# Performance work log

Measured on AMD Instinct MI355X. Metric: run time of the kernel, lower is better.

## Reference

```python
import jax, jax.numpy as jnp
import numpy as np

B, LQ, LK, QD, KD, VD, H = 8, 128, 1024, 128, 128, 128, 128
NEG_INF = -1e6  # d2l masked_softmax fill value


def setup_inputs() -> dict:
    key = jax.random.key(0)
    k1, k2, k3, k4, k5, k6, k7 = jax.random.split(key, 7)
    return {
        "queries": jax.random.normal(k1, (B, LQ, QD), dtype=jnp.float32),
        "keys": jax.random.normal(k2, (B, LK, KD), dtype=jnp.float32),
        "values": jax.random.normal(k3, (B, LK, VD), dtype=jnp.float32),
        "valid_lens": jax.random.randint(k4, (B,), 0, LK),
        # learned params: torch Linear(in,out,bias=False); stored here as [in,out]
        "W_q": jax.random.normal(k5, (QD, H), dtype=jnp.float32) / np.sqrt(QD),
        "W_k": jax.random.normal(k6, (KD, H), dtype=jnp.float32) / np.sqrt(KD),
        "w_v": jax.random.normal(k7, (H,), dtype=jnp.float32) / np.sqrt(H),
    }


def reference(queries, keys, values, valid_lens, W_q, W_k, w_v):
    q = jnp.einsum("blq,qh->blh", queries, W_q)            # [B,Lq,H]
    k = jnp.einsum("bsk,kh->bsh", keys, W_k)               # [B,Lk,H]
    features = jnp.tanh(q[:, :, None, :] + k[:, None, :, :])  # [B,Lq,Lk,H]
    scores = jnp.einsum("blsh,h->bls", features, w_v)      # [B,Lq,Lk]
    mask = jnp.arange(LK)[None, None, :] < valid_lens[:, None, None]
    scores = jnp.where(mask, scores, NEG_INF)
    attn = jax.nn.softmax(scores, axis=-1)                 # dropout p=0.0 -> identity
    return jnp.einsum("bls,bsv->blv", attn, values)        # [B,Lq,Vd]
```

## Files before the change

### kernel.cpp

```cpp
#include <hip/hip_runtime.h>
#include <hip/hip_fp16.h>

#define B_   8
#define LQ_  128
#define LK_  1024
#define H_   128

__device__ float        g_eq  [B_ * LQ_ * H_];
__device__ uint4        g_ekT4[B_ * (H_ / 4) * (LK_ / 2)];
__device__ unsigned int g_vh  [B_ * LK_ * (H_ / 2)];

#define C2LOG2E 2.8853900817779268f

__global__ __launch_bounds__(256) void proj_conv(const float* __restrict__ q,
                                                 const float* __restrict__ k,
                                                 const float* __restrict__ Wq,
                                                 const float* __restrict__ Wk,
                                                 const float* __restrict__ values) {
    const int bx = blockIdx.x, ch = blockIdx.y;
    const int t = threadIdx.x;
    if (bx >= 288) {
        const int idx = ((bx - 288) + (ch << 9)) * 256 + t;
        float4 v = *(const float4*)(values + (size_t)idx * 4);
        __half2 p0 = __floats2half2_rn(v.x, v.y);
        __half2 p1 = __floats2half2_rn(v.z, v.w);
        *(uint2*)(g_vh + (size_t)idx * 2) =
            make_uint2(*(unsigned int*)&p0, *(unsigned int*)&p1);
        return;
    }
    __shared__ float Ws[H_ * 64];
    __shared__ float Xs[32 * H_];
    const bool isq = (bx < 32);
    const float* X; const float* W; int r0;
    if (isq) { X = q; W = Wq; r0 = bx * 32; }
    else     { X = k; W = Wk; r0 = (bx - 32) * 32; }

    #pragma unroll
    for (int u = 0; u < 8; ++u) {
        int p = u * 256 + t;
        int kk = p >> 4, c4 = p & 15;
        *(float4*)(Ws + kk * 64 + c4 * 4) = *(const float4*)(W + kk * H_ + ch * 64 + c4 * 4);
    }
    #pragma unroll
    for (int u = 0; u < 4; ++u) {
        int idx = u * 256 + t;
        int r = idx >> 5, c = idx & 31;
        *(float4*)(Xs + r * H_ + c * 4) = *(const float4*)(X + (size_t)(r0 + r) * H_ + c * 4);
    }
    __syncthreads();

    const int rr = t >> 4;
    const int cc = t & 15;
    float acc[2][4] = {};
    #pragma unroll 4
    for (int kk = 0; kk < H_; ++kk) {
        float4 w4 = *(const float4*)(Ws + kk * 64 + cc * 4);
        float x0 = Xs[(rr * 2) * H_ + kk];
        float x1 = Xs[(rr * 2 + 1) * H_ + kk];
        acc[0][0] = fmaf(x0, w4.x, acc[0][0]); acc[0][1] = fmaf(x0, w4.y, acc[0][1]);
        acc[0][2] = fmaf(x0, w4.z, acc[0][2]); acc[0][3] = fmaf(x0, w4.w, acc[0][3]);
        acc[1][0] = fmaf(x1, w4.x, acc[1][0]); acc[1][1] = fmaf(x1, w4.y, acc[1][1]);
        acc[1][2] = fmaf(x1, w4.z, acc[1][2]); acc[1][3] = fmaf(x1, w4.w, acc[1][3]);
    }
    if (isq) {
        #pragma unroll
        for (int i = 0; i < 2; ++i) {
            float4 o;
            o.x = __builtin_amdgcn_exp2f(acc[i][0] * C2LOG2E);
            o.y = __builtin_amdgcn_exp2f(acc[i][1] * C2LOG2E);
            o.z = __builtin_amdgcn_exp2f(acc[i][2] * C2LOG2E);
            o.w = __builtin_amdgcn_exp2f(acc[i][3] * C2LOG2E);
            *(float4*)(g_eq + (size_t)(r0 + rr * 2 + i) * H_ + ch * 64 + cc * 4) = o;
        }
    } else {
        const int b  = r0 >> 10;
        const int s0 = (r0 & 1023) + rr * 2;
        const int h4 = ch * 16 + cc;
        uint4 pk;
        #pragma unroll
        for (int j = 0; j < 4; ++j) {
            float e0 = __builtin_amdgcn_exp2f(acc[0][j] * C2LOG2E);
            float e1 = __builtin_amdgcn_exp2f(acc[1][j] * C2LOG2E);
            __half2 p = __floats2half2_rn(e0, e1);
            ((unsigned int*)&pk)[j] = *(unsigned int*)&p;
        }
        g_ekT4[((size_t)b * (H_ / 4) + h4) * (LK_ / 2) + (s0 >> 1)] = pk;
    }
}

__global__ __launch_bounds__(512, 4) void fused_attn(const int* __restrict__ valid_lens,
                                                     const float* __restrict__ w_v,
                                                     float* __restrict__ out) {
    __shared__ float scA[LK_], scB[LK_];
    __shared__ float sredA[8], sredB[8];
    __shared__ float rinvs[2];
    __shared__ float part[16][2][H_];
    const int t = threadIdx.x;
    const int lane = t & 63, wid = t >> 6;
    const int b = blockIdx.x >> 6, l0 = (blockIdx.x & 63) * 2;
    int valid = valid_lens[b];
    valid = min(max(valid, 0), LK_);

    const int s0 = 2 * t;
    float p0 = 0.0f, p1 = 0.0f;
    if (valid == 0) {
        for (int i = t; i < LK_; i += 512) { scA[i] = 1.0f; scB[i] = 1.0f; }
    } else if (s0 < valid) {
        const float* __restrict__ q0 = g_eq + (size_t)(b * LQ_ + l0) * H_;
        const float* __restrict__ q1 = q0 + H_;
        const uint4* __restrict__ ek = g_ekT4 + (size_t)b * (H_ / 4) * (LK_ / 2) + t;
        float a00 = 0.0f, a01 = 0.0f, a10 = 0.0f, a11 = 0.0f;
        #pragma unroll
        for (int hb = 0; hb < 4; ++hb) {
            uint4 r[8];
            #pragma unroll
            for (int i = 0; i < 8; ++i)
                r[i] = ek[(size_t)(hb * 8 + i) * (LK_ / 2)];
            #pragma unroll
            for (int i = 0; i < 8; ++i) {
                #pragma unroll
                for (int j = 0; j < 4; ++j) {
                    unsigned int uj = ((const unsigned int*)&r[i])[j];
                    float2 ef = __half22float2(*(const __half2*)&uj);
                    const int h = (hb * 8 + i) * 4 + j;
                    const float qa = q0[h], qb = q1[h], wh = w_v[h];
                    a00 = fmaf(wh, __builtin_amdgcn_rcpf(fmaf(qa, ef.x, 1.0f)), a00);
                    a01 = fmaf(wh, __builtin_amdgcn_rcpf(fmaf(qa, ef.y, 1.0f)), a01);
                    a10 = fmaf(wh, __builtin_amdgcn_rcpf(fmaf(qb, ef.x, 1.0f)), a10);
                    a11 = fmaf(wh, __builtin_amdgcn_rcpf(fmaf(qb, ef.y, 1.0f)), a11);
                }
            }
        }
        const float c = -2.0f * 1.44269504f;
        float e00 = __builtin_amdgcn_exp2f(a00 * c);
        float e01 = __builtin_amdgcn_exp2f(a01 * c);
        float e10 = __builtin_amdgcn_exp2f(a10 * c);
        float e11 = __builtin_amdgcn_exp2f(a11 * c);
        *(float2*)(scA + s0) = make_float2(e00, e01);
        *(float2*)(scB + s0) = make_float2(e10, e11);
        const bool odd_ok = (s0 + 1 < valid);
        p0 = e00 + (odd_ok ? e01 : 0.0f);
        p1 = e10 + (odd_ok ? e11 : 0.0f);
    }
    #pragma unroll
    for (int kk = 32; kk; kk >>= 1) {
        p0 += __shfl_xor(p0, kk, 64);
        p1 += __shfl_xor(p1, kk, 64);
    }
    if (lane == 0) { sredA[wid] = p0; sredB[wid] = p1; }
    __syncthreads();
    if (t < 2) {
        const float* sr = t ? sredB : sredA;
        float s8 = ((sr[0] + sr[1]) + (sr[2] + sr[3]))
                 + ((sr[4] + sr[5]) + (sr[6] + sr[7]));
        rinvs[t] = (valid == 0) ? (1.0f / 1024.0f) : (1.0f / s8);
    }
    __syncthreads();
    const int n = (valid == 0) ? LK_ : valid;

    const int c = t >> 5;
    const int v4 = t & 31;
    const uint2* vb = (const uint2*)g_vh + (size_t)b * LK_ * (H_ / 4) + v4;
    float ax0 = 0.0f, ay0 = 0.0f, az0 = 0.0f, aw0 = 0.0f;
    float ax1 = 0.0f, ay1 = 0.0f, az1 = 0.0f, aw1 = 0.0f;
    int s = c;
    for (; s + 16 * 7 < n; s += 16 * 8) {
        uint2 r[8];
        #pragma unroll
        for (int i = 0; i < 8; ++i)
            r[i] = vb[(size_t)(s + 16 * i) * (H_ / 4)];
        #pragma unroll
        for (int i = 0; i < 8; ++i) {
            float2 v01 = __half22float2(*(const __half2*)&r[i].x);
            float2 v23 = __half22float2(*(const __half2*)&r[i].y);
            float w0 = scA[s + 16 * i], w1 = scB[s + 16 * i];
            ax0 = fmaf(w0, v01.x, ax0); ay0 = fmaf(w0, v01.y, ay0);
            az0 = fmaf(w0, v23.x, az0); aw0 = fmaf(w0, v23.y, aw0);
            ax1 = fmaf(w1, v01.x, ax1); ay1 = fmaf(w1, v01.y, ay1);
            az1 = fmaf(w1, v23.x, az1); aw1 = fmaf(w1, v23.y, aw1);
        }
    }
    for (; s < n; s += 16) {
        uint2 u = vb[(size_t)s * (H_ / 4)];
        float2 v01 = __half22float2(*(const __half2*)&u.x);
        float2 v23 = __half22float2(*(const __half2*)&u.y);
        float w0 = scA[s], w1 = scB[s];
        ax0 = fmaf(w0, v01.x, ax0); ay0 = fmaf(w0, v01.y, ay0);
        az0 = fmaf(w0, v23.x, az0); aw0 = fmaf(w0, v23.y, aw0);
        ax1 = fmaf(w1, v01.x, ax1); ay1 = fmaf(w1, v01.y, ay1);
        az1 = fmaf(w1, v23.x, az1); aw1 = fmaf(w1, v23.y, aw1);
    }
    *(float4*)(&part[c][0][4 * v4]) = make_float4(ax0, ay0, az0, aw0);
    *(float4*)(&part[c][1][4 * v4]) = make_float4(ax1, ay1, az1, aw1);
    __syncthreads();
    if (t < 256) {
        const int rr = t >> 7, v = t & 127;
        float o = 0.0f;
        #pragma unroll
        for (int cc2 = 0; cc2 < 16; ++cc2) o += part[cc2][rr][v];
        out[(b * LQ_ + l0 + rr) * H_ + v] = o * rinvs[rr];
    }
}

extern "C" void kernel_launch(void* const* d_in, const int* in_sizes, int n_in,
                              void* d_out, int out_size, void* d_ws, size_t ws_size,
                              hipStream_t stream) {
    const float* queries    = (const float*)d_in[0];
    const float* keys       = (const float*)d_in[1];
    const float* values     = (const float*)d_in[2];
    const int*   valid_lens = (const int*)d_in[3];
    const float* W_q        = (const float*)d_in[4];
    const float* W_k        = (const float*)d_in[5];
    const float* w_v        = (const float*)d_in[6];
    float* out = (float*)d_out;
    (void)d_ws; (void)ws_size; (void)in_sizes; (void)n_in; (void)out_size;

    proj_conv <<<dim3(800, 2), 256, 0, stream>>>(queries, keys, W_q, W_k, values);
    fused_attn<<<512, 512, 0, stream>>>(valid_lens, w_v, out);
}
```

Baseline: 34.31 us.

## Stage query/w_v rows in LDS, interleave batch-to-block mapping, simplify unrolled loops

Loads the two query rows and w_v into shared memory once per block instead of reading them from global memory inside the inner score loop. Remaps block indices so adjacent blocks alternate between two halves of the batch, which should spread blocks with different valid lengths across the GPU more evenly. Replaces the manual 8-deep load batching in both loops with simpler loops using unroll 4, and lowers the min-blocks launch bound from 4 to 2. The result is less memory-level parallelism per thread and a different register budget, traded for fewer redundant loads and better load balance.

```diff
diff --git a/kernel.cpp b/kernel.cpp
--- a/kernel.cpp
+++ b/kernel.cpp
@@ -88,54 +88,55 @@
     }
 }
 
-__global__ __launch_bounds__(512, 4) void fused_attn(const int* __restrict__ valid_lens,
+__global__ __launch_bounds__(512, 2) void fused_attn(const int* __restrict__ valid_lens,
                                                      const float* __restrict__ w_v,
                                                      float* __restrict__ out) {
+    __shared__ float qs[2][H_];
+    __shared__ float wv[H_];
     __shared__ float scA[LK_], scB[LK_];
     __shared__ float sredA[8], sredB[8];
     __shared__ float rinvs[2];
     __shared__ float part[16][2][H_];
     const int t = threadIdx.x;
     const int lane = t & 63, wid = t >> 6;
-    const int b = blockIdx.x >> 6, l0 = (blockIdx.x & 63) * 2;
+    const int g = blockIdx.x & 1;
+    const int idx = blockIdx.x >> 1;
+    const int b = 4 * g + (idx & 3);
+    const int l0 = (idx >> 2) * 2;
     int valid = valid_lens[b];
     valid = min(max(valid, 0), LK_);
+
+    if (t < 256) qs[t >> 7][t & 127] = g_eq[(size_t)(b * LQ_ + l0 + (t >> 7)) * H_ + (t & 127)];
+    else if (t < 384) wv[t - 256] = w_v[t - 256];
+    __syncthreads();
 
     const int s0 = 2 * t;
     float p0 = 0.0f, p1 = 0.0f;
     if (valid == 0) {
         for (int i = t; i < LK_; i += 512) { scA[i] = 1.0f; scB[i] = 1.0f; }
     } else if (s0 < valid) {
-        const float* __restrict__ q0 = g_eq + (size_t)(b * LQ_ + l0) * H_;
-        const float* __restrict__ q1 = q0 + H_;
         const uint4* __restrict__ ek = g_ekT4 + (size_t)b * (H_ / 4) * (LK_ / 2) + t;
         float a00 = 0.0f, a01 = 0.0f, a10 = 0.0f, a11 = 0.0f;
-        #pragma unroll
-        for (int hb = 0; hb < 4; ++hb) {
-            uint4 r[8];
+        #pragma unroll 4
+        for (int h4 = 0; h4 < H_ / 4; ++h4) {
+            uint4 u = ek[(size_t)h4 * (LK_ / 2)];
             #pragma unroll
-            for (int i = 0; i < 8; ++i)
-                r[i] = ek[(size_t)(hb * 8 + i) * (LK_ / 2)];
-            #pragma unroll
-            for (int i = 0; i < 8; ++i) {
-                #pragma unroll
-                for (int j = 0; j < 4; ++j) {
-                    unsigned int uj = ((const unsigned int*)&r[i])[j];
-                    float2 ef = __half22float2(*(const __half2*)&uj);
-                    const int h = (hb * 8 + i) * 4 + j;
-                    const float qa = q0[h], qb = q1[h], wh = w_v[h];
-                    a00 = fmaf(wh, __builtin_amdgcn_rcpf(fmaf(qa, ef.x, 1.0f)), a00);
-                    a01 = fmaf(wh, __builtin_amdgcn_rcpf(fmaf(qa, ef.y, 1.0f)), a01);
-                    a10 = fmaf(wh, __builtin_amdgcn_rcpf(fmaf(qb, ef.x, 1.0f)), a10);
-                    a11 = fmaf(wh, __builtin_amdgcn_rcpf(fmaf(qb, ef.y, 1.0f)), a11);
-                }
+            for (int j = 0; j < 4; ++j) {
+                unsigned int uj = ((const unsigned int*)&u)[j];
+                float2 ef = __half22float2(*(const __half2*)&uj);
+                const int h = h4 * 4 + j;
+                const float qa = qs[0][h], qb = qs[1][h], wh = wv[h];
+                a00 = fmaf(wh, __builtin_amdgcn_rcpf(fmaf(qa, ef.x, 1.0f)), a00);
+                a01 = fmaf(wh, __builtin_amdgcn_rcpf(fmaf(qa, ef.y, 1.0f)), a01);
+                a10 = fmaf(wh, __builtin_amdgcn_rcpf(fmaf(qb, ef.x, 1.0f)), a10);
+                a11 = fmaf(wh, __builtin_amdgcn_rcpf(fmaf(qb, ef.y, 1.0f)), a11);
             }
         }
-        const float c = -2.0f * 1.44269504f;
-        float e00 = __builtin_amdgcn_exp2f(a00 * c);
-        float e01 = __builtin_amdgcn_exp2f(a01 * c);
-        float e10 = __builtin_amdgcn_exp2f(a10 * c);
-        float e11 = __builtin_amdgcn_exp2f(a11 * c);
+        const float cc = -2.0f * 1.44269504f;
+        float e00 = __builtin_amdgcn_exp2f(a00 * cc);
+        float e01 = __builtin_amdgcn_exp2f(a01 * cc);
+        float e10 = __builtin_amdgcn_exp2f(a10 * cc);
+        float e11 = __builtin_amdgcn_exp2f(a11 * cc);
         *(float2*)(scA + s0) = make_float2(e00, e01);
         *(float2*)(scB + s0) = make_float2(e10, e11);
         const bool odd_ok = (s0 + 1 < valid);
@@ -163,24 +164,8 @@
     const uint2* vb = (const uint2*)g_vh + (size_t)b * LK_ * (H_ / 4) + v4;
     float ax0 = 0.0f, ay0 = 0.0f, az0 = 0.0f, aw0 = 0.0f;
     float ax1 = 0.0f, ay1 = 0.0f, az1 = 0.0f, aw1 = 0.0f;
-    int s = c;
-    for (; s + 16 * 7 < n; s += 16 * 8) {
-        uint2 r[8];
-        #pragma unroll
-        for (int i = 0; i < 8; ++i)
-            r[i] = vb[(size_t)(s + 16 * i) * (H_ / 4)];
-        #pragma unroll
-        for (int i = 0; i < 8; ++i) {
-            float2 v01 = __half22float2(*(const __half2*)&r[i].x);
-            float2 v23 = __half22float2(*(const __half2*)&r[i].y);
-            float w0 = scA[s + 16 * i], w1 = scB[s + 16 * i];
-            ax0 = fmaf(w0, v01.x, ax0); ay0 = fmaf(w0, v01.y, ay0);
-            az0 = fmaf(w0, v23.x, az0); aw0 = fmaf(w0, v23.y, aw0);
-            ax1 = fmaf(w1, v01.x, ax1); ay1 = fmaf(w1, v01.y, ay1);
-            az1 = fmaf(w1, v23.x, az1); aw1 = fmaf(w1, v23.y, aw1);
-        }
-    }
-    for (; s < n; s += 16) {
+    #pragma unroll 4
+    for (int s = c; s < n; s += 16) {
         uint2 u = vb[(size_t)s * (H_ / 4)];
         float2 v01 = __half22float2(*(const __half2*)&u.x);
         float2 v23 = __half22float2(*(const __half2*)&u.y);
@@ -198,7 +183,7 @@
         float o = 0.0f;
         #pragma unroll
         for (int cc2 = 0; cc2 < 16; ++cc2) o += part[cc2][rr][v];
-        out[(b * LQ_ + l0 + rr) * H_ + v] = o * rinvs[rr];
+        out[(size_t)(b * LQ_ + l0 + rr) * H_ + v] = o * rinvs[rr];
     }
 }
 
```

Result: slower. 36.97 us (+7.8%).
